# Kernel optimization log

Hardware: AMD Instinct MI355X
Metric: run time of the kernel (lower is better)

Reference implementation:

```python
import math
import jax, jax.numpy as jnp
import numpy as np

# module constants (mirror __init__ with m=5, n=2, groups=4, dilation=2)
M = 5                       # Taylor order param
N = 2
U = 1 + 2 ** (N - 1)        # unit_FZ = 3
GROUPS = 4
DIL = 2                     # self.dilation
BOUNDARY = math.sqrt(math.ceil((M - 1) / 2))  # sqrt(2)
KSIZE = U * (M - 1) + 1     # 13


def _pad_to(t, T):
    """pad_num: center-pad last dim up to length T (extra on the right if odd)."""
    d = T - t.shape[-1]
    return jnp.pad(t, [(0, 0), (0, 0), (d // 2, d - d // 2)])


def setup_inputs() -> dict:
    key = jax.random.key(0)
    k1, k2, k3 = jax.random.split(key, 3)
    B, C, T = 8, 256, 16384
    O = 256
    fan_in = (C // GROUPS) * KSIZE
    x = jax.random.normal(k1, (B, C, T), dtype=jnp.float32)
    w = jax.random.normal(k2, (O, C // GROUPS, KSIZE), dtype=jnp.float32) / math.sqrt(fan_in)
    b = jax.random.normal(k3, (O,), dtype=jnp.float32) / math.sqrt(fan_in)
    return {"x": x, "w": w, "b": b}


def reference(x, w, b):
    B, C, T = x.shape
    O = w.shape[0]
    out = jnp.zeros((B, O, T), dtype=x.dtype)
    for i in range(DIL):
        xs = x[:, :, i::DIL]                      # (B, C, Ti)
        Ti = xs.shape[-1]
        # zero-insertion (stride-U upsample) fused into the conv via lhs_dilation,
        # grouped conv1d with padding U-1 on both sides
        y = jax.lax.conv_general_dilated(
            xs, w, window_strides=(1,), padding=[(U - 1, U - 1)],
            lhs_dilation=(U,), rhs_dilation=(1,),
            dimension_numbers=("NCH", "OIH", "NCH"),
            feature_group_count=GROUPS,
        ) + b[None, :, None]                      # (B, O, Lout)
        lst = []
        # j == 0: base term + detached neighbor-difference denominator
        t0 = _pad_to(y[:, :, U - 1::U], Ti)       # (B, O, Ti)
        lst.append(t0)
        t0d = jax.lax.stop_gradient(t0)
        pl = (M - 1) // 2
        pr = (M - 1) - pl
        padded = jnp.pad(t0d, [(0, 0), (0, 0), (pl, pr)])
        # windows[b,c,k,t] = padded[b,c,t+k]  (size-M time neighborhood)
        win = jnp.stack([padded[:, :, k:k + Ti] for k in range(M)], axis=2)  # (B,O,M,Ti)
        denom = jnp.clip((t0d[:, :, None, :] - win).mean(axis=2), 1.0, BOUNDARY)
        # j >= 1: strided finite differences
        for j in range(1, U):
            d = y[:, :, j - 1 + U::U] - y[:, :, :-U][:, :, j - 1::U]
            lst.append(_pad_to(d, Ti) / denom)
        # recursive log2-depth higher-order combination
        if len(lst) > 2:
            n_order = math.floor(math.log2(len(lst) - 1)) + 1
            ro = 2
            while ro <= n_order:
                cal = lst[-2 ** (n_order - ro + 1):]
                for k in range(2 ** (n_order - ro)):
                    xk = cal[2 ** (n_order - ro) + k] - cal[2 ** (n_order - ro) - k - 1]
                    xk = xk / (2 ** (n_order - ro))
                    lst.append(_pad_to(math.factorial(ro) * xk, Ti) / denom)
                ro += 1
        dia = jnp.mean(jnp.stack(lst, axis=0), axis=0)  # (B, O, Ti)
        out = out.at[:, :, i::DIL].set(dia)
    return out
```

## Files before the change

kernel.cpp:

```cpp
#include <hip/hip_runtime.h>
#include <hip/hip_bf16.h>


typedef float v4f __attribute__((ext_vector_type(4)));
typedef short v8s __attribute__((ext_vector_type(8)));

#define TI 8192
#define TFULL 16384
#define TB 76
#define NTILE 108
#define XPH_BYTES 10752
#define RES_S 77
#define LDS_BYTES 39424

__device__ __forceinline__ unsigned bf16w(float f) {
    unsigned u = __float_as_uint(f);
    return (u + 0x7FFFu + ((u >> 16) & 1u)) >> 16;
}

__device__ __forceinline__ unsigned packbf2(float lo, float hi) {
    union { __hip_bfloat162 h; unsigned u; } cv;
    cv.h = __float22bfloat162_rn(make_float2(lo, hi));
    return cv.u;
}

__global__ void prep_kernel(const float* __restrict__ w, unsigned short* __restrict__ gw) {
    int id = blockIdx.x * 256 + threadIdx.x;
    int j    = id & 7;
    int lane = (id >> 3) & 63;
    int fid  = id >> 9;
    int mt   = fid % 12;  fid /= 12;
    int kc   = fid & 1;   fid >>= 1;
    int e    = fid % 5;
    int g    = fid / 5;
    int a  = mt >> 2;
    int mg = mt & 3;
    int o  = 16 * mg + (lane & 15);
    int c  = 32 * kc + (lane >> 4) * 8 + j;
    const float* wb = w + (((size_t)(g * 64 + o)) * 64 + c) * 13;
    float val;
    if (a == 0) {
        val = wb[3 * e];
    } else {
        int tap = (a == 1) ? 1 : 2;
        float lo = (e > 0) ? wb[3 * (e - 1) + tap] : 0.0f;
        float hi = (e < 4) ? wb[3 * e + tap] : 0.0f;
        val = lo - hi;
    }
    gw[id] = (unsigned short)bf16w(val);
}

__global__ __launch_bounds__(512, 4)
void pconv_mfma(const unsigned short* __restrict__ gw, const float* __restrict__ x,
                const float* __restrict__ bias, float* __restrict__ out) {
    extern __shared__ char smem[];
    float* smemf = (float*)smem;

    const int tid  = threadIdx.x;
    const int lane = tid & 63;
    const int wv   = tid >> 6;
    const int mg   = wv >> 1;
    const int ph   = wv & 1;
    const int col  = lane & 15;
    const int quad = lane >> 4;

    const int tileIdx = blockIdx.x;
    const int g       = blockIdx.y;
    const int b       = blockIdx.z;
    const int tb      = tileIdx * TB;

    {
        const float* xb = x + ((size_t)(b * 256 + g * 64)) * TFULL;
        const int v0 = 2 * tb - 8;
        for (int f = tid; f < 1344; f += 512) {
            int q  = f % 42;
            int cp = f / 42;
            int vq = v0 + 4 * q;
            const float* r0 = xb + (size_t)(2 * cp) * TFULL;
            const float* r1 = r0 + TFULL;
            float a0, a1, a2, a3, b0, b1, b2, b3;
            if (vq >= 0 && vq + 3 < TFULL) {
                v4f A4 = *(const v4f*)(r0 + vq);
                v4f B4 = *(const v4f*)(r1 + vq);
                a0 = A4[0]; a1 = A4[1]; a2 = A4[2]; a3 = A4[3];
                b0 = B4[0]; b1 = B4[1]; b2 = B4[2]; b3 = B4[3];
            } else {
                a0 = (vq >= 0 && vq < TFULL) ? r0[vq] : 0.0f;
                a1 = (vq + 1 >= 0 && vq + 1 < TFULL) ? r0[vq + 1] : 0.0f;
                a2 = (vq + 2 >= 0 && vq + 2 < TFULL) ? r0[vq + 2] : 0.0f;
                a3 = (vq + 3 >= 0 && vq + 3 < TFULL) ? r0[vq + 3] : 0.0f;
                b0 = (vq >= 0 && vq < TFULL) ? r1[vq] : 0.0f;
                b1 = (vq + 1 >= 0 && vq + 1 < TFULL) ? r1[vq + 1] : 0.0f;
                b2 = (vq + 2 >= 0 && vq + 2 < TFULL) ? r1[vq + 2] : 0.0f;
                b3 = (vq + 3 >= 0 && vq + 3 < TFULL) ? r1[vq + 3] : 0.0f;
            }
            int cblk = cp >> 2;
            int woff = (cp & 3) * 4;
            unsigned w0 = packbf2(a0, b0);
            unsigned w1 = packbf2(a1, b1);
            unsigned w2 = packbf2(a2, b2);
            unsigned w3 = packbf2(a3, b3);
            int t0r = 2 * q, t1r = 2 * q + 1;
            *(unsigned*)(smem + 0 * XPH_BYTES + t0r * 128 + ((cblk ^ (t0r & 7)) << 4) + woff) = w0;
            *(unsigned*)(smem + 1 * XPH_BYTES + t0r * 128 + ((cblk ^ (t0r & 7)) << 4) + woff) = w1;
            *(unsigned*)(smem + 0 * XPH_BYTES + t1r * 128 + ((cblk ^ (t1r & 7)) << 4) + woff) = w2;
            *(unsigned*)(smem + 1 * XPH_BYTES + t1r * 128 + ((cblk ^ (t1r & 7)) << 4) + woff) = w3;
        }
    }
    __syncthreads();

    const unsigned short* gwp = gw + (size_t)g * 61440;
    v4f acc[3][5];
    #pragma unroll
    for (int a = 0; a < 3; ++a)
        #pragma unroll
        for (int u = 0; u < 5; ++u) acc[a][u] = (v4f){0.f, 0.f, 0.f, 0.f};

    const char* xph = smem + ph * XPH_BYTES;
    #pragma unroll
    for (int e = 0; e < 5; ++e) {
        #pragma unroll
        for (int kc = 0; kc < 2; ++kc) {
            v8s Af[3];
            #pragma unroll
            for (int a = 0; a < 3; ++a)
                Af[a] = *(const v8s*)(gwp + (((e * 2 + kc) * 12 + 4 * a + mg) << 9) + (lane << 3));
            const int sw = (col + e) * 128 + (((4 * kc + quad) ^ ((col + e) & 7)) << 4);
            #pragma unroll
            for (int u = 0; u < 5; ++u) {
                v8s Bf = *(const v8s*)(xph + u * 2048 + sw);
                #pragma unroll
                for (int a = 0; a < 3; ++a)
                    acc[a][u] = __builtin_amdgcn_mfma_f32_16x16x32_bf16(Bf, Af[a], acc[a][u], 0, 0, 0);
            }
        }
    }

    const int oL = 16 * mg + col;
    const float bias_s = bias[g * 64 + oL];
    const bool edge = (tileIdx == 0) || (tileIdx == NTILE - 1);

    #pragma unroll
    for (int u = 0; u < 5; ++u) {
        v4f t0v = acc[0][u];
        #pragma unroll
        for (int r = 0; r < 4; ++r) t0v[r] += bias_s;
        if (edge) {
            v4f d2v = acc[1][u];
            v4f d1v = acc[2][u];
            #pragma unroll
            for (int r = 0; r < 4; ++r) {
                int t = tb - 2 + 16 * u + 4 * quad + r;
                if (t < 2 || t > TI - 3) { t0v[r] = 0.f; d2v[r] = 0.f; d1v[r] = 0.f; }
            }
            acc[1][u] = d2v;
            acc[2][u] = d1v;
        }
        acc[0][u] = t0v;
    }

    __syncthreads();

    float* resp = smemf + ph * (64 * RES_S);
    const int tlb = (lane + 48) & 63;
    const int tla = (lane + 16) & 63;
    #pragma unroll
    for (int u = 0; u < 5; ++u) {
        const v4f Tm = acc[0][u];
        const v4f Tp = acc[0][u > 0 ? u - 1 : 0];
        const v4f Tn = acc[0][u < 4 ? u + 1 : 4];
        float b2o = __shfl(Tm[2], tlb), b2s = __shfl(Tp[2], tlb);
        float b1o = __shfl(Tm[3], tlb), b1s = __shfl(Tp[3], tlb);
        float a0o = __shfl(Tm[0], tla), a0s = __shfl(Tn[0], tla);
        float a1o = __shfl(Tm[1], tla), a1s = __shfl(Tn[1], tla);
        float wn[8];
        wn[0] = (quad == 0) ? b2s : b2o;
        wn[1] = (quad == 0) ? b1s : b1o;
        wn[2] = Tm[0]; wn[3] = Tm[1]; wn[4] = Tm[2]; wn[5] = Tm[3];
        wn[6] = (quad == 3) ? a0s : a0o;
        wn[7] = (quad == 3) ? a1s : a1o;
        #pragma unroll
        for (int r = 0; r < 4; ++r) {
            float t0 = wn[r + 2];
            float m5 = 0.2f * (wn[r] + wn[r + 1] + wn[r + 2] + wn[r + 3] + wn[r + 4]);
            float den = fminf(fmaxf(t0 - m5, 1.0f), 1.41421356237309515f);
            float rc = 1.0f / den;
            float d2 = acc[1][u][r];
            float d1 = acc[2][u][r];
            float res = 0.25f * (t0 + (d1 + d2) * rc + 2.0f * (d2 - d1) * rc * rc);
            int j = 16 * u + 4 * quad + r - 2;
            if (j >= 0 && j < TB) resp[oL * RES_S + j] = res;
        }
    }
    __syncthreads();

    const float* r0b = smemf;
    const float* r1b = smemf + 64 * RES_S;
    float* obase = out + ((size_t)(b * 256 + g * 64)) * TFULL;
    const int jmax = (tb + TB <= TI) ? TB : (TI - tb);
    #pragma unroll
    for (int it = 0; it < 10; ++it) {
        int f = tid + it * 512;
        if (f < 64 * TB) {
            int j = f % TB;
            int o = f / TB;
            if (j < jmax) {
                float2 v;
                v.x = r0b[o * RES_S + j];
                v.y = r1b[o * RES_S + j];
                *(float2*)(obase + (size_t)o * TFULL + 2 * (tb + j)) = v;
            }
        }
    }
}

extern "C" void kernel_launch(void* const* d_in, const int* in_sizes, int n_in,
                              void* d_out, int out_size, void* d_ws, size_t ws_size,
                              hipStream_t stream) {
    const float* x  = (const float*)d_in[0];
    const float* w  = (const float*)d_in[1];
    const float* bb = (const float*)d_in[2];
    float* out = (float*)d_out;

    unsigned short* gw = (unsigned short*)d_ws;

    prep_kernel<<<960, 256, 0, stream>>>(w, gw);
    pconv_mfma<<<dim3(NTILE, 4, 8), 512, LDS_BYTES, stream>>>(gw, x, bb, out);
}
```

Measured before the change: 302.6 us.

## Restructure load/store indexing, split result LDS region, add setprio and swizzle tweak

Gives each thread a fixed channel pair for the input staging loop, so division by 42 goes away and bounds checks are skipped on interior tiles. The XOR swizzle key changes from the time row to the row pair, and the staging writes are regrouped to match. The result buffer moves to a separate LDS region, which removes a __syncthreads between the MFMA phase and the epilogue, but it raises LDS per block from about 39KB to 61KB and may lower occupancy. It also raises wave priority around the MFMA loop and rewrites the output store as per-wave row loops without divisions.

```diff
diff --git a/kernel.cpp b/kernel.cpp
--- a/kernel.cpp
+++ b/kernel.cpp
@@ -10,8 +10,9 @@
 #define TB 76
 #define NTILE 108
 #define XPH_BYTES 10752
+#define RES_F 5376
 #define RES_S 77
-#define LDS_BYTES 39424
+#define LDS_BYTES 60928
 
 __device__ __forceinline__ unsigned bf16w(float f) {
     unsigned u = __float_as_uint(f);
@@ -68,18 +69,24 @@
     const int g       = blockIdx.y;
     const int b       = blockIdx.z;
     const int tb      = tileIdx * TB;
+    const bool interiorT = (tileIdx > 0) && (tileIdx < NTILE - 1);
 
     {
         const float* xb = x + ((size_t)(b * 256 + g * 64)) * TFULL;
         const int v0 = 2 * tb - 8;
-        for (int f = tid; f < 1344; f += 512) {
-            int q  = f % 42;
-            int cp = f / 42;
+        const int cp   = tid >> 4;
+        const int qlo  = tid & 15;
+        const int cblk = cp >> 2;
+        const int woff = (cp & 3) * 4;
+        const float* r0 = xb + (size_t)(2 * cp) * TFULL;
+        const float* r1 = r0 + TFULL;
+        #pragma unroll
+        for (int it = 0; it < 3; ++it) {
+            if (it == 2 && qlo >= 10) continue;
+            int q  = qlo + 16 * it;
             int vq = v0 + 4 * q;
-            const float* r0 = xb + (size_t)(2 * cp) * TFULL;
-            const float* r1 = r0 + TFULL;
             float a0, a1, a2, a3, b0, b1, b2, b3;
-            if (vq >= 0 && vq + 3 < TFULL) {
+            if (interiorT) {
                 v4f A4 = *(const v4f*)(r0 + vq);
                 v4f B4 = *(const v4f*)(r1 + vq);
                 a0 = A4[0]; a1 = A4[1]; a2 = A4[2]; a3 = A4[3];
@@ -94,17 +101,16 @@
                 b2 = (vq + 2 >= 0 && vq + 2 < TFULL) ? r1[vq + 2] : 0.0f;
                 b3 = (vq + 3 >= 0 && vq + 3 < TFULL) ? r1[vq + 3] : 0.0f;
             }
-            int cblk = cp >> 2;
-            int woff = (cp & 3) * 4;
             unsigned w0 = packbf2(a0, b0);
             unsigned w1 = packbf2(a1, b1);
             unsigned w2 = packbf2(a2, b2);
             unsigned w3 = packbf2(a3, b3);
-            int t0r = 2 * q, t1r = 2 * q + 1;
-            *(unsigned*)(smem + 0 * XPH_BYTES + t0r * 128 + ((cblk ^ (t0r & 7)) << 4) + woff) = w0;
-            *(unsigned*)(smem + 1 * XPH_BYTES + t0r * 128 + ((cblk ^ (t0r & 7)) << 4) + woff) = w1;
-            *(unsigned*)(smem + 0 * XPH_BYTES + t1r * 128 + ((cblk ^ (t1r & 7)) << 4) + woff) = w2;
-            *(unsigned*)(smem + 1 * XPH_BYTES + t1r * 128 + ((cblk ^ (t1r & 7)) << 4) + woff) = w3;
+            int sel = ((cblk ^ (q & 7)) << 4) + woff;
+            char* base0 = smem + sel + (2 * q) * 128;
+            *(unsigned*)(base0)                   = w0;
+            *(unsigned*)(base0 + 128)             = w2;
+            *(unsigned*)(base0 + XPH_BYTES)       = w1;
+            *(unsigned*)(base0 + XPH_BYTES + 128) = w3;
         }
     }
     __syncthreads();
@@ -117,6 +123,7 @@
         for (int u = 0; u < 5; ++u) acc[a][u] = (v4f){0.f, 0.f, 0.f, 0.f};
 
     const char* xph = smem + ph * XPH_BYTES;
+    __builtin_amdgcn_s_setprio(1);
     #pragma unroll
     for (int e = 0; e < 5; ++e) {
         #pragma unroll
@@ -125,7 +132,7 @@
             #pragma unroll
             for (int a = 0; a < 3; ++a)
                 Af[a] = *(const v8s*)(gwp + (((e * 2 + kc) * 12 + 4 * a + mg) << 9) + (lane << 3));
-            const int sw = (col + e) * 128 + (((4 * kc + quad) ^ ((col + e) & 7)) << 4);
+            const int sw = (col + e) * 128 + (((4 * kc + quad) ^ (((col + e) >> 1) & 7)) << 4);
             #pragma unroll
             for (int u = 0; u < 5; ++u) {
                 v8s Bf = *(const v8s*)(xph + u * 2048 + sw);
@@ -135,17 +142,17 @@
             }
         }
     }
+    __builtin_amdgcn_s_setprio(0);
 
     const int oL = 16 * mg + col;
     const float bias_s = bias[g * 64 + oL];
-    const bool edge = (tileIdx == 0) || (tileIdx == NTILE - 1);
 
     #pragma unroll
     for (int u = 0; u < 5; ++u) {
         v4f t0v = acc[0][u];
         #pragma unroll
         for (int r = 0; r < 4; ++r) t0v[r] += bias_s;
-        if (edge) {
+        if (!interiorT) {
             v4f d2v = acc[1][u];
             v4f d1v = acc[2][u];
             #pragma unroll
@@ -159,9 +166,7 @@
         acc[0][u] = t0v;
     }
 
-    __syncthreads();
-
-    float* resp = smemf + ph * (64 * RES_S);
+    float* resp = smemf + RES_F + ph * (64 * RES_S);
     const int tlb = (lane + 48) & 63;
     const int tla = (lane + 16) & 63;
     #pragma unroll
@@ -194,22 +199,24 @@
     }
     __syncthreads();
 
-    const float* r0b = smemf;
-    const float* r1b = smemf + 64 * RES_S;
+    const float* r0b = smemf + RES_F;
+    const float* r1b = r0b + 64 * RES_S;
     float* obase = out + ((size_t)(b * 256 + g * 64)) * TFULL;
-    const int jmax = (tb + TB <= TI) ? TB : (TI - tb);
-    #pragma unroll
-    for (int it = 0; it < 10; ++it) {
-        int f = tid + it * 512;
-        if (f < 64 * TB) {
-            int j = f % TB;
-            int o = f / TB;
-            if (j < jmax) {
-                float2 v;
-                v.x = r0b[o * RES_S + j];
-                v.y = r1b[o * RES_S + j];
-                *(float2*)(obase + (size_t)o * TFULL + 2 * (tb + j)) = v;
-            }
+    #pragma unroll
+    for (int i = 0; i < 8; ++i) {
+        int o = 8 * wv + i;
+        const float* rr0 = r0b + o * RES_S;
+        const float* rr1 = r1b + o * RES_S;
+        float* op = obase + (size_t)o * TFULL + 2 * (size_t)tb;
+        int j = lane;
+        if (tb + j < TI) {
+            float2 v; v.x = rr0[j]; v.y = rr1[j];
+            *(float2*)(op + 2 * j) = v;
+        }
+        j = 64 + lane;
+        if (j < TB && tb + j < TI) {
+            float2 v; v.x = rr0[j]; v.y = rr1[j];
+            *(float2*)(op + 2 * j) = v;
         }
     }
 }
```

Result: no change. 302.1 us (-0.2%).
